# Performance work log

Measured on AMD Instinct MI355X. Metric: run time of the kernel, lower is better.

The kernel has to match this reference:

```python
import jax, jax.numpy as jnp
import numpy as np

N_NODES = 100000
N_EDGES = 1250000
IN_CH = 128
OUT_CH = 64


def setup_inputs() -> dict:
    key = jax.random.key(0)
    k1, k2, k3, k4 = jax.random.split(key, 4)
    x = jax.random.normal(k1, (N_NODES, IN_CH), dtype=jnp.float32)
    edge_index = jax.random.randint(k2, (2, N_EDGES), 0, N_NODES, dtype=jnp.int64)
    edge_weight = jax.random.uniform(k3, (N_EDGES,), dtype=jnp.float32)
    # Xavier-uniform weight, zero bias (as in reset_parameters)
    limit = float(np.sqrt(6.0 / (IN_CH + OUT_CH)))
    W = jax.random.uniform(k4, (IN_CH, OUT_CH), dtype=jnp.float32, minval=-limit, maxval=limit)
    b = jnp.zeros((OUT_CH,), dtype=jnp.float32)
    return {"x": x, "edge_index": edge_index, "edge_weight": edge_weight, "W": W, "b": b}


def reference(x, edge_index, edge_weight, W, b):
    # Dense transform: [N, in] @ [in, out] -> [N, out]
    h = jnp.matmul(x, W)
    row, col = edge_index[0], edge_index[1]
    n = h.shape[0]
    # Weighted in-degree via scatter-add on destination (row)
    deg = jnp.zeros((n,), dtype=h.dtype).at[row].add(edge_weight)
    # deg^-0.5 with inf (deg==0) replaced by 0
    deg_inv_sqrt = jnp.where(deg == 0, jnp.zeros_like(deg), deg ** -0.5)
    norm = deg_inv_sqrt[row] * deg_inv_sqrt[col]  # [E]
    # Gather source features, normalize, scatter-add to destinations
    out = jnp.zeros_like(h).at[row].add(h[col] * norm[:, None])
    return out + b
```

## Files before the change

kernel.cpp:

```cpp
#include <hip/hip_runtime.h>

#define N_NODES 100000
#define N_EDGES 1250000
#define IN_CH 128
#define OUT_CH 64

#define NPB 128
#define ACCS 65
#define NBINS 782
#define BINCAP_DEF 2048
#define NB1 256
#define B1T 512
#define CH1 ((N_EDGES + NB1 - 1) / NB1)
#define MAXU ((CH1 + B1T - 1) / B1T)
#define CURS_STRIDE 16

#define EXP20 0x0A000000u
#define INV_SCALE_ACC 9.5367431640625e-07f
#define SCALE_DEG 33554432.0f
#define INV_SCALE_DEG 2.9802322387695312e-08f

typedef __attribute__((ext_vector_type(8))) short short8;
typedef __attribute__((ext_vector_type(4))) float f32x4;

__device__ inline unsigned int f2bf(float f) {
    unsigned int u = __float_as_uint(f);
    unsigned int r = ((u >> 16) & 1u) + 0x7FFFu;
    return (u + r) >> 16;
}
__device__ inline float bf_lo(unsigned int p) { return __uint_as_float(p << 16); }
__device__ inline float bf_hi(unsigned int p) { return __uint_as_float(p & 0xFFFF0000u); }

__device__ inline int qlo(unsigned int p, unsigned int k) {
    return (int)__uint_as_float((p << 16) + k);
}
__device__ inline int qhi(unsigned int p, unsigned int k) {
    return (int)__uint_as_float((p & 0xFFFF0000u) + k);
}

__global__ __launch_bounds__(256) void wbconv_kernel(const float* __restrict__ W,
                                                     unsigned int* __restrict__ Wb,
                                                     int* __restrict__ cursor,
                                                     int bincap) {
    int g = blockIdx.x * 256 + threadIdx.x;
    if (g < NBINS) cursor[g * CURS_STRIDE] = g * bincap;

    int c = g >> 8;
    int t = (g >> 6) & 3;
    int l = g & 63;
    int q = l >> 4, r15 = l & 15;
    unsigned int o[4];
#pragma unroll
    for (int jj = 0; jj < 4; ++jj) {
        float f0 = W[(c * 32 + q * 8 + 2 * jj)     * OUT_CH + t * 16 + r15];
        float f1 = W[(c * 32 + q * 8 + 2 * jj + 1) * OUT_CH + t * 16 + r15];
        o[jj] = f2bf(f0) | (f2bf(f1) << 16);
    }
    *(uint4*)(Wb + (size_t)g * 4) = make_uint4(o[0], o[1], o[2], o[3]);
}

__global__ __launch_bounds__(B1T) void bin1_kernel(const int* __restrict__ ei,
                                                   const float* __restrict__ ew,
                                                   int* __restrict__ cursor,
                                                   int2* __restrict__ brec,
                                                   int bincap) {
    __shared__ int hist[NBINS];
    __shared__ int base[NBINS];
    __shared__ int rank[NBINS];
    const int t = threadIdx.x;
    for (int i = t; i < NBINS; i += B1T) { hist[i] = 0; rank[i] = 0; }
    __syncthreads();

    const int e0 = blockIdx.x * CH1;
    const int e1 = (e0 + CH1 < N_EDGES) ? e0 + CH1 : N_EDGES;

    int rowv[MAXU], colv[MAXU];
    float wv[MAXU];
#pragma unroll
    for (int u = 0; u < MAXU; ++u) {
        int e = e0 + t + u * B1T;
        bool ok = e < e1;
        rowv[u] = ok ? ei[e] : -1;
        colv[u] = ok ? ei[N_EDGES + e] : 0;
        wv[u]   = ok ? ew[e] : 0.0f;
        if (ok) atomicAdd(&hist[rowv[u] >> 7], 1);
    }
    __syncthreads();

    for (int i = t; i < NBINS; i += B1T)
        if (hist[i] > 0) base[i] = atomicAdd(&cursor[i * CURS_STRIDE], hist[i]);
    __syncthreads();

#pragma unroll
    for (int u = 0; u < MAXU; ++u) {
        if (rowv[u] >= 0) {
            int b = rowv[u] >> 7;
            int rk = atomicAdd(&rank[b], 1);
            int idx = base[b] + rk;
            if (idx < (b + 1) * bincap)
                brec[idx] = make_int2(((rowv[u] & 127) << 17) | colv[u],
                                      __float_as_int(wv[u]));
        }
    }
}

__global__ __launch_bounds__(256) void bin2_kernel(const int* __restrict__ cursor,
                                                   const int2* __restrict__ brec,
                                                   float* __restrict__ dis_g,
                                                   int bincap) {
    __shared__ int deg[NPB];
    const int t = threadIdx.x;
    const int b = blockIdx.x;
    if (t < NPB) deg[t] = 0;
    __syncthreads();

    const int rbase = b * bincap;
    int m = cursor[b * CURS_STRIDE] - rbase;
    if (m > bincap) m = bincap;

    for (int j = t; j < m; j += 256) {
        int2 rec = brec[rbase + j];
        atomicAdd(&deg[rec.x >> 17], __float2int_rn(__int_as_float(rec.y) * SCALE_DEG));
    }
    __syncthreads();

    int node = b * NPB + t;
    if (t < NPB && node < N_NODES) {
        float d = (float)deg[t] * INV_SCALE_DEG;
        dis_g[node] = (d == 0.0f) ? 0.0f : (1.0f / sqrtf(d));
    }
}

__global__ __launch_bounds__(256) void gemm_kernel(const float* __restrict__ x,
                                                   const unsigned int* __restrict__ Wb,
                                                   const float* __restrict__ dis,
                                                   unsigned int* __restrict__ hs) {
    const int tid  = threadIdx.x;
    const int w    = tid >> 6;
    const int lane = tid & 63;
    const int q    = lane >> 4, r15 = lane & 15;
    const int node = blockIdx.x * 64 + w * 16 + r15;
    const int nl   = (node < N_NODES) ? node : N_NODES - 1;
    const float* xrow = x + (size_t)nl * IN_CH;

    f32x4 acc[4];
#pragma unroll
    for (int t = 0; t < 4; ++t) acc[t] = (f32x4){0.f, 0.f, 0.f, 0.f};

#pragma unroll
    for (int c = 0; c < 4; ++c) {
        float4 xa = *(const float4*)(xrow + c * 32 + q * 8);
        float4 xb = *(const float4*)(xrow + c * 32 + q * 8 + 4);
        short8 bfrag;
        bfrag[0] = (short)f2bf(xa.x); bfrag[1] = (short)f2bf(xa.y);
        bfrag[2] = (short)f2bf(xa.z); bfrag[3] = (short)f2bf(xa.w);
        bfrag[4] = (short)f2bf(xb.x); bfrag[5] = (short)f2bf(xb.y);
        bfrag[6] = (short)f2bf(xb.z); bfrag[7] = (short)f2bf(xb.w);
#pragma unroll
        for (int t = 0; t < 4; ++t) {
            short8 afrag = *(const short8*)(Wb + (size_t)((c * 4 + t) * 64 + lane) * 4);
            acc[t] = __builtin_amdgcn_mfma_f32_16x16x32_bf16(afrag, bfrag, acc[t], 0, 0, 0);
        }
    }

    if (node < N_NODES) {
        float di = dis[node];
#pragma unroll
        for (int t = 0; t < 4; ++t) {
            unsigned int p0 = f2bf(acc[t][0] * di) | (f2bf(acc[t][1] * di) << 16);
            unsigned int p1 = f2bf(acc[t][2] * di) | (f2bf(acc[t][3] * di) << 16);
            *(uint2*)(hs + (size_t)node * 32 + t * 8 + q * 2) = make_uint2(p0, p1);
        }
    }
}

__global__ __launch_bounds__(512) void bingather_kernel(const int* __restrict__ cursor,
                                                        const int2* __restrict__ brec,
                                                        const uint4* __restrict__ hs,
                                                        const float* __restrict__ dis,
                                                        const float* __restrict__ b,
                                                        float* __restrict__ out,
                                                        int bincap) {
    __shared__ int acc[NPB * ACCS];
    const int t = threadIdx.x;
    const int blk = blockIdx.x;
    for (int k = t; k < NPB * ACCS; k += 512) acc[k] = 0;
    __syncthreads();

    const int rbase = blk * bincap;
    int m = cursor[blk * CURS_STRIDE] - rbase;
    if (m > bincap) m = bincap;

    const int wid = t >> 6, lane = t & 63;
    const int sub = lane >> 3, l8 = lane & 7;
    const unsigned int K = EXP20;

    for (int j0 = wid * 16; j0 < m; j0 += 128) {
        int jA = j0 + sub;
        int jB = j0 + 8 + sub;
        bool okA = jA < m, okB = jB < m;
        int recA = okA ? brec[rbase + jA].x : 0;
        int recB = okB ? brec[rbase + jB].x : 0;
        uint4 pA = make_uint4(0, 0, 0, 0), pB = make_uint4(0, 0, 0, 0);
        if (okA) pA = hs[(size_t)(recA & 0x1FFFF) * 8 + l8];
        if (okB) pB = hs[(size_t)(recB & 0x1FFFF) * 8 + l8];
        if (okA) {
            int ba = (recA >> 17) * ACCS + 8 * l8;
            atomicAdd(&acc[ba + 0], qlo(pA.x, K)); atomicAdd(&acc[ba + 1], qhi(pA.x, K));
            atomicAdd(&acc[ba + 2], qlo(pA.y, K)); atomicAdd(&acc[ba + 3], qhi(pA.y, K));
            atomicAdd(&acc[ba + 4], qlo(pA.z, K)); atomicAdd(&acc[ba + 5], qhi(pA.z, K));
            atomicAdd(&acc[ba + 6], qlo(pA.w, K)); atomicAdd(&acc[ba + 7], qhi(pA.w, K));
        }
        if (okB) {
            int bb = (recB >> 17) * ACCS + 8 * l8;
            atomicAdd(&acc[bb + 0], qlo(pB.x, K)); atomicAdd(&acc[bb + 1], qhi(pB.x, K));
            atomicAdd(&acc[bb + 2], qlo(pB.y, K)); atomicAdd(&acc[bb + 3], qhi(pB.y, K));
            atomicAdd(&acc[bb + 4], qlo(pB.z, K)); atomicAdd(&acc[bb + 5], qhi(pB.z, K));
            atomicAdd(&acc[bb + 6], qlo(pB.w, K)); atomicAdd(&acc[bb + 7], qhi(pB.w, K));
        }
    }
    __syncthreads();

    float bc = b[lane];
#pragma unroll 4
    for (int r = 0; r < 16; ++r) {
        int nl = wid * 16 + r;
        int node = blk * NPB + nl;
        if (node < N_NODES) {
            float di = dis[node] * INV_SCALE_ACC;
            out[(size_t)node * OUT_CH + lane] = (float)acc[nl * ACCS + lane] * di + bc;
        }
    }
}

extern "C" void kernel_launch(void* const* d_in, const int* in_sizes, int n_in,
                              void* d_out, int out_size, void* d_ws, size_t ws_size,
                              hipStream_t stream) {
    const float* x  = (const float*)d_in[0];
    const int*   ei = (const int*)d_in[1];
    const float* ew = (const float*)d_in[2];
    const float* W  = (const float*)d_in[3];
    const float* b  = (const float*)d_in[4];
    float* out = (float*)d_out;

    unsigned int* hs = (unsigned int*)d_ws;
    unsigned int* Wb = hs + (size_t)N_NODES * 32;
    int*   cursor  = (int*)(Wb + 4096);
    float* dis     = (float*)(cursor + NBINS * CURS_STRIDE);
    int2*  brec    = (int2*)(dis + N_NODES);
    size_t used = (size_t)N_NODES * 32 + 4096 + (size_t)NBINS * CURS_STRIDE
                + (size_t)N_NODES;
    size_t rem  = (ws_size / 4 > used) ? ws_size / 4 - used : 0;
    int bincap  = (int)(rem / (2 * (size_t)NBINS));
    if (bincap > BINCAP_DEF) bincap = BINCAP_DEF;

    wbconv_kernel<<<4, 256, 0, stream>>>(W, Wb, cursor, bincap);
    bin1_kernel<<<NB1, B1T, 0, stream>>>(ei, ew, cursor, brec, bincap);
    bin2_kernel<<<NBINS, 256, 0, stream>>>(cursor, brec, dis, bincap);
    gemm_kernel<<<(N_NODES + 63) / 64, 256, 0, stream>>>(x, Wb, dis, hs);
    bingather_kernel<<<NBINS, 512, 0, stream>>>(cursor, brec, (const uint4*)hs,
                                                dis, b, out, bincap);
}
```

Measured before the change: 167.3 us.

## Pack two biased fixed-point channels into one 64-bit LDS atomic add

Replaces the per-channel 32-bit LDS integer atomics with 64-bit atomics that each carry two channels. Each channel is quantized to fixed point with a positive bias so the low half never borrows into the high half. A per-node edge counter is kept so the bias can be subtracted during the epilogue. This halves the number of LDS atomic operations in the gather. In exchange it uses a coarser quantization scale, risks overflow if the bias times the edge count gets large, and adds float conversions per element.

Measured after the change: 164.0 us. Within noise of the previous version (-2.0%).

```diff
diff --git a/kernel.cpp b/kernel.cpp
--- a/kernel.cpp
+++ b/kernel.cpp
@@ -6,7 +6,7 @@
 #define OUT_CH 64
 
 #define NPB 128
-#define ACCS 65
+#define ACCS2 33
 #define NBINS 782
 #define BINCAP_DEF 2048
 #define NB1 256
@@ -15,8 +15,10 @@
 #define MAXU ((CH1 + B1T - 1) / B1T)
 #define CURS_STRIDE 16
 
-#define EXP20 0x0A000000u
-#define INV_SCALE_ACC 9.5367431640625e-07f
+#define QSCALE 8192.0f
+#define QBIAS_F 16777216.0f
+#define QBIAS_U 16777216u
+#define INV_QSCALE 1.220703125e-4f
 #define SCALE_DEG 33554432.0f
 #define INV_SCALE_DEG 2.9802322387695312e-08f
 
@@ -31,11 +33,10 @@
 __device__ inline float bf_lo(unsigned int p) { return __uint_as_float(p << 16); }
 __device__ inline float bf_hi(unsigned int p) { return __uint_as_float(p & 0xFFFF0000u); }
 
-__device__ inline int qlo(unsigned int p, unsigned int k) {
-    return (int)__uint_as_float((p << 16) + k);
-}
-__device__ inline int qhi(unsigned int p, unsigned int k) {
-    return (int)__uint_as_float((p & 0xFFFF0000u) + k);
+__device__ inline unsigned long long qpack(unsigned int p) {
+    unsigned int lo = (unsigned int)__float2int_rn(fmaf(bf_lo(p), QSCALE, QBIAS_F));
+    unsigned int hi = (unsigned int)__float2int_rn(fmaf(bf_hi(p), QSCALE, QBIAS_F));
+    return ((unsigned long long)hi << 32) | (unsigned long long)lo;
 }
 
 __global__ __launch_bounds__(256) void wbconv_kernel(const float* __restrict__ W,
@@ -181,10 +182,12 @@
                                                         const float* __restrict__ b,
                                                         float* __restrict__ out,
                                                         int bincap) {
-    __shared__ int acc[NPB * ACCS];
+    __shared__ unsigned long long acc[NPB * ACCS2];
+    __shared__ int cnt[NPB];
     const int t = threadIdx.x;
     const int blk = blockIdx.x;
-    for (int k = t; k < NPB * ACCS; k += 512) acc[k] = 0;
+    for (int k = t; k < NPB * ACCS2; k += 512) acc[k] = 0ull;
+    if (t < NPB) cnt[t] = 0;
     __syncthreads();
 
     const int rbase = blk * bincap;
@@ -193,7 +196,6 @@
 
     const int wid = t >> 6, lane = t & 63;
     const int sub = lane >> 3, l8 = lane & 7;
-    const unsigned int K = EXP20;
 
     for (int j0 = wid * 16; j0 < m; j0 += 128) {
         int jA = j0 + sub;
@@ -205,30 +207,36 @@
         if (okA) pA = hs[(size_t)(recA & 0x1FFFF) * 8 + l8];
         if (okB) pB = hs[(size_t)(recB & 0x1FFFF) * 8 + l8];
         if (okA) {
-            int ba = (recA >> 17) * ACCS + 8 * l8;
-            atomicAdd(&acc[ba + 0], qlo(pA.x, K)); atomicAdd(&acc[ba + 1], qhi(pA.x, K));
-            atomicAdd(&acc[ba + 2], qlo(pA.y, K)); atomicAdd(&acc[ba + 3], qhi(pA.y, K));
-            atomicAdd(&acc[ba + 4], qlo(pA.z, K)); atomicAdd(&acc[ba + 5], qhi(pA.z, K));
-            atomicAdd(&acc[ba + 6], qlo(pA.w, K)); atomicAdd(&acc[ba + 7], qhi(pA.w, K));
+            int ba = (recA >> 17) * ACCS2 + 4 * l8;
+            atomicAdd(&acc[ba + 0], qpack(pA.x));
+            atomicAdd(&acc[ba + 1], qpack(pA.y));
+            atomicAdd(&acc[ba + 2], qpack(pA.z));
+            atomicAdd(&acc[ba + 3], qpack(pA.w));
+            if (l8 == 0) atomicAdd(&cnt[recA >> 17], 1);
         }
         if (okB) {
-            int bb = (recB >> 17) * ACCS + 8 * l8;
-            atomicAdd(&acc[bb + 0], qlo(pB.x, K)); atomicAdd(&acc[bb + 1], qhi(pB.x, K));
-            atomicAdd(&acc[bb + 2], qlo(pB.y, K)); atomicAdd(&acc[bb + 3], qhi(pB.y, K));
-            atomicAdd(&acc[bb + 4], qlo(pB.z, K)); atomicAdd(&acc[bb + 5], qhi(pB.z, K));
-            atomicAdd(&acc[bb + 6], qlo(pB.w, K)); atomicAdd(&acc[bb + 7], qhi(pB.w, K));
-        }
-    }
-    __syncthreads();
-
+            int bb = (recB >> 17) * ACCS2 + 4 * l8;
+            atomicAdd(&acc[bb + 0], qpack(pB.x));
+            atomicAdd(&acc[bb + 1], qpack(pB.y));
+            atomicAdd(&acc[bb + 2], qpack(pB.z));
+            atomicAdd(&acc[bb + 3], qpack(pB.w));
+            if (l8 == 0) atomicAdd(&cnt[recB >> 17], 1);
+        }
+    }
+    __syncthreads();
+
+    const unsigned int* acc32 = (const unsigned int*)acc;
     float bc = b[lane];
+    int half = lane & 1, slot = lane >> 1;
 #pragma unroll 4
     for (int r = 0; r < 16; ++r) {
         int nl = wid * 16 + r;
         int node = blk * NPB + nl;
         if (node < N_NODES) {
-            float di = dis[node] * INV_SCALE_ACC;
-            out[(size_t)node * OUT_CH + lane] = (float)acc[nl * ACCS + lane] * di + bc;
+            unsigned int raw = acc32[(nl * ACCS2 + slot) * 2 + half];
+            int qsum = (int)(raw - (unsigned int)cnt[nl] * QBIAS_U);
+            float di = dis[node] * INV_QSCALE;
+            out[(size_t)node * OUT_CH + lane] = (float)qsum * di + bc;
         }
     }
 }
```
